# Performance work log

Measured on AMD Instinct MI355X. Metric: run time of the kernel, lower is better.

Reference implementation:

```python
import jax, jax.numpy as jnp
import numpy as np

N_EMBD = 1024
N_HEAD = 16
B, T = 4, 2048


def setup_inputs() -> dict:
    key = jax.random.key(0)
    ks = jax.random.split(key, 4)
    s = 1.0 / np.sqrt(N_EMBD)
    return {
        "x": jax.random.normal(ks[0], (B, T, N_EMBD), dtype=jnp.float32),
        "w_attn": jax.random.normal(ks[1], (N_EMBD, 3 * N_EMBD), dtype=jnp.float32) * s,
        "b_attn": jnp.zeros((3 * N_EMBD,), dtype=jnp.float32),
        "w_proj": jax.random.normal(ks[2], (N_EMBD, N_EMBD), dtype=jnp.float32) * s,
        "b_proj": jnp.zeros((N_EMBD,), dtype=jnp.float32),
    }


def reference(x, w_attn, b_attn, w_proj, b_proj):
    Bb, Tt, C = x.shape
    H = N_HEAD
    D = C // H  # head dim
    qkv = x @ w_attn + b_attn  # [B,T,3C]
    q, k, v = jnp.split(qkv, 3, axis=2)
    # [B,H,T,D]
    q = q.reshape(Bb, Tt, H, D).transpose(0, 2, 1, 3)
    k = k.reshape(Bb, Tt, H, D).transpose(0, 2, 1, 3)
    v = v.reshape(Bb, Tt, H, D).transpose(0, 2, 1, 3)
    scale = 1.0 / np.sqrt(D).astype(np.float32)
    attn = jnp.einsum("bhqd,bhkd->bhqk", q, k) * scale
    mask = jnp.tril(jnp.ones((Tt, Tt), dtype=bool))
    attn = jnp.where(mask, attn, jnp.float32(-jnp.inf))
    probs = jax.nn.softmax(attn, axis=-1)
    out = jnp.einsum("bhqk,bhkd->bhqd", probs, v)
    out = out.transpose(0, 2, 1, 3).reshape(Bb, Tt, C)
    return out @ w_proj + b_proj
```

## Files before the change

kernel.cpp:

```cpp
#include <hip/hip_runtime.h>
#include <hip/hip_bf16.h>


typedef float f32x4 __attribute__((ext_vector_type(4)));
typedef float f32x16 __attribute__((ext_vector_type(16)));
typedef short short8 __attribute__((ext_vector_type(8)));
typedef short short4v __attribute__((ext_vector_type(4)));

__device__ __forceinline__ short f2bf(float f) {
  union { __hip_bfloat16 h; short s; } u;
  u.h = __float2bfloat16(f);
  return u.s;
}

__device__ __forceinline__ void gl_lds16(const void* g, void* l) {
  __builtin_amdgcn_global_load_lds(
      (const __attribute__((address_space(1))) void*)g,
      (__attribute__((address_space(3))) void*)l, 16, 0, 0);
}

__global__ void prep(const float* __restrict__ x, const float* __restrict__ wa,
                     const float* __restrict__ wp, short* __restrict__ xb,
                     short* __restrict__ wat, short* __restrict__ wpt) {
  const int bid = blockIdx.x, tid = threadIdx.x;
  if (bid < 8192) {
    int i = (bid * 256 + tid) * 4;
    float4 v = *(const float4*)(x + i);
    short4v o;
    o[0] = f2bf(v.x); o[1] = f2bf(v.y); o[2] = f2bf(v.z); o[3] = f2bf(v.w);
    *(short4v*)(xb + i) = o;
    return;
  }
  __shared__ float tile[32][33];
  const float* in;
  short* out;
  int N, bx, by;
  if (bid < 11264) {
    int t = bid - 8192;
    in = wa; out = wat; N = 3072; bx = t % 96; by = t / 96;
  } else {
    int t = bid - 11264;
    in = wp; out = wpt; N = 1024; bx = t & 31; by = t >> 5;
  }
  int tx = tid & 31, ty = tid >> 5;
  int x0 = bx * 32, y0 = by * 32;
#pragma unroll
  for (int i = 0; i < 32; i += 8)
    tile[ty + i][tx] = in[(size_t)(y0 + ty + i) * N + x0 + tx];
  __syncthreads();
#pragma unroll
  for (int i = 0; i < 32; i += 8)
    out[(size_t)(x0 + ty + i) * 1024 + y0 + tx] = f2bf(tile[tx][ty + i]);
}

#define GEMM_BODY(A_, Bt_)                                                        \
  __shared__ __align__(16) short As[128 * 32];                                    \
  __shared__ __align__(16) short Bs[128 * 32];                                    \
  const int tid = threadIdx.x;                                                    \
  const int wv = tid >> 6;                                                        \
  const int wr = wv >> 1, wc = wv & 1;                                            \
  const int col = tid & 31, khalf = (tid >> 5) & 1;                               \
  const int m0 = blockIdx.y * 128, n0 = blockIdx.x * 128;                         \
  f32x16 acc[2][2];                                                               \
  _Pragma("unroll") for (int i = 0; i < 2; ++i)                                   \
      _Pragma("unroll") for (int j = 0; j < 2; ++j)                               \
          acc[i][j] = (f32x16)(0.f);                                              \
  for (int k0 = 0; k0 < 1024; k0 += 32) {                                         \
    _Pragma("unroll") for (int i = 0; i < 2; ++i) {                               \
      int cc = tid + i * 256;                                                     \
      int row = cc >> 2, part = ((cc & 3) - ((cc >> 3) & 3)) & 3;                 \
      gl_lds16(A_ + (size_t)(m0 + row) * 1024 + k0 + part * 8,                    \
               (char*)As + cc * 16);                                              \
      gl_lds16(Bt_ + (size_t)(n0 + row) * 1024 + k0 + part * 8,                   \
               (char*)Bs + cc * 16);                                              \
    }                                                                             \
    __syncthreads();                                                              \
    short8 af[2][2], bf[2][2];                                                    \
    _Pragma("unroll") for (int i = 0; i < 2; ++i)                                 \
        _Pragma("unroll") for (int s = 0; s < 2; ++s) {                           \
          int pa = s * 2 + khalf;                                                 \
          int ra = wr * 64 + i * 32 + col;                                        \
          int rb = wc * 64 + i * 32 + col;                                        \
          af[i][s] = *(const short8*)&As[(ra * 4 + ((pa + (ra >> 1)) & 3)) * 8];  \
          bf[i][s] = *(const short8*)&Bs[(rb * 4 + ((pa + (rb >> 1)) & 3)) * 8];  \
        }                                                                         \
    _Pragma("unroll") for (int s = 0; s < 2; ++s)                                 \
        _Pragma("unroll") for (int i = 0; i < 2; ++i)                             \
            _Pragma("unroll") for (int j = 0; j < 2; ++j)                         \
                acc[i][j] = __builtin_amdgcn_mfma_f32_32x32x16_bf16(              \
                    af[i][s], bf[j][s], acc[i][j], 0, 0, 0);                      \
    __syncthreads();                                                              \
  }

__global__ __launch_bounds__(256, 2) void gemm_proj(
    const short* __restrict__ A, const short* __restrict__ Bt,
    const float* __restrict__ bias, float* __restrict__ out) {
  GEMM_BODY(A, Bt)
  const int rhalf = khalf * 4;
#pragma unroll
  for (int i = 0; i < 2; ++i) {
#pragma unroll
    for (int j = 0; j < 2; ++j) {
      int n = n0 + wc * 64 + j * 32 + col;
      float bv = bias[n];
      int mb = m0 + wr * 64 + i * 32 + rhalf;
#pragma unroll
      for (int a = 0; a < 16; ++a) {
        int m = mb + (a & 3) + 8 * (a >> 2);
        out[(size_t)m * 1024 + n] = acc[i][j][a] + bv;
      }
    }
  }
}


#define BARRIER() asm volatile("s_barrier" ::: "memory")
#define VMC(N) asm volatile("s_waitcnt vmcnt(" #N ")" ::: "memory")

#define STG(KT, S, SRC, LB)                                                \
  if ((KT) < 16) {                                                         \
    char* db_ = (char*)(LB) + (((KT) & 1) ? 32768 : 0) + ((S) * 16384);    \
    const short* sb_ = (SRC) + (KT) * 64 + (S) * 32;                       \
    gl_lds16(sb_ + g_off0, db_ + d_off0);                                  \
    gl_lds16(sb_ + g_off1, db_ + d_off1);                                  \
  }

#define LDF(AF, BF, ABP, BBP, S, AO, BO)                                   \
  _Pragma("unroll") for (int mt_ = 0; mt_ < 4; ++mt_)                      \
      AF[mt_] = *(const short8*)((ABP) + (S) * 16384 + (AO)[mt_]);         \
  _Pragma("unroll") for (int nt_ = 0; nt_ < 2; ++nt_)                      \
      BF[nt_] = *(const short8*)((BBP) + (S) * 16384 + (BO)[nt_]);

#define MFMA8_BODY(AF, BF)                                                 \
  __builtin_amdgcn_s_setprio(1);                                           \
  _Pragma("unroll") for (int mt_ = 0; mt_ < 4; ++mt_)                      \
      _Pragma("unroll") for (int nt_ = 0; nt_ < 2; ++nt_)                  \
          acc[mt_][nt_] = __builtin_amdgcn_mfma_f32_32x32x16_bf16(         \
              AF[mt_], BF[nt_], acc[mt_][nt_], 0, 0, 0);                   \
  __builtin_amdgcn_s_setprio(0);

#define MFMA8(AF, BF)                                                      \
  __builtin_amdgcn_sched_barrier(0);                                       \
  asm volatile("s_waitcnt lgkmcnt(6)" ::: "memory");                       \
  MFMA8_BODY(AF, BF)

#define MFMA8_LG0(AF, BF)                                                  \
  __builtin_amdgcn_sched_barrier(0);                                       \
  asm volatile("s_waitcnt lgkmcnt(0)" ::: "memory");                       \
  MFMA8_BODY(AF, BF)

__global__ __launch_bounds__(512, 2) void gemm_qkv(
    const short* __restrict__ A, const short* __restrict__ Bt,
    const float* __restrict__ bias, short* __restrict__ Qb,
    short* __restrict__ Kb, short* __restrict__ Vtb) {
  __shared__ __align__(16) short Asm[2][16384];
  __shared__ __align__(16) short Bsm[2][16384];
  const int tid = threadIdx.x;
  const int wv = tid >> 6;
  const int wr = wv >> 2, wc = wv & 3;
  const int ln32 = tid & 31, khalf = (tid >> 5) & 1;
  const int m0 = blockIdx.y * 256, n0 = blockIdx.x * 256;

  const int d_off0 = tid * 16, d_off1 = d_off0 + 8192;
  const int pa_st = ((tid & 3) - ((tid >> 3) & 3)) & 3;
  const size_t g_off0 = (size_t)(tid >> 2) * 1024 + (size_t)pa_st * 8;
  const size_t g_off1 = g_off0 + (size_t)128 * 1024;

  const int rot = (ln32 >> 1) & 3;
  const int slotE = (khalf + rot) & 3;
  const int slotO = (2 + khalf + rot) & 3;
  int aoffE[4], aoffO[4], boffE[2], boffO[2];
#pragma unroll
  for (int mt = 0; mt < 4; ++mt) {
    int r = (wr * 128 + mt * 32 + ln32) * 64;
    aoffE[mt] = r + slotE * 16;
    aoffO[mt] = r + slotO * 16;
  }
#pragma unroll
  for (int nt = 0; nt < 2; ++nt) {
    int r = (wc * 64 + nt * 32 + ln32) * 64;
    boffE[nt] = r + slotE * 16;
    boffO[nt] = r + slotO * 16;
  }

  const short* srcA = A + (size_t)m0 * 1024;
  const short* srcB = Bt + (size_t)n0 * 1024;

  f32x16 acc[4][2];
#pragma unroll
  for (int i = 0; i < 4; ++i)
#pragma unroll
    for (int j = 0; j < 2; ++j) acc[i][j] = (f32x16)(0.f);

  short8 af0[4], af1[4], bf0[2], bf1[2];

  STG(0, 0, srcA, Asm)
  STG(0, 0, srcB, Bsm)
  STG(0, 1, srcA, Asm)
  STG(0, 1, srcB, Bsm)
  STG(1, 0, srcA, Asm)
  STG(1, 0, srcB, Bsm)
  VMC(4);
  BARRIER();
  {
    const char* Ab0 = (const char*)Asm;
    const char* Bb0 = (const char*)Bsm;
    LDF(af0, bf0, Ab0, Bb0, 0, aoffE, boffE)
  }

  for (int kt = 0; kt < 16; ++kt) {
    const char* Ab = (const char*)Asm + ((kt & 1) << 15);
    const char* Bb = (const char*)Bsm + ((kt & 1) << 15);
    const char* An = (const char*)Asm + (((kt + 1) & 1) << 15);
    const char* Bn = (const char*)Bsm + (((kt + 1) & 1) << 15);
    LDF(af1, bf1, Ab, Bb, 0, aoffO, boffO)
    STG(kt + 1, 1, srcA, Asm)
    MFMA8(af0, bf0)
    LDF(af0, bf0, Ab, Bb, 1, aoffE, boffE)
    STG(kt + 1, 1, srcB, Bsm)
    MFMA8(af1, bf1)
    if (kt == 15) { VMC(0); } else { VMC(4); }
    BARRIER();
    LDF(af1, bf1, Ab, Bb, 1, aoffO, boffO)
    STG(kt + 2, 0, srcA, Asm)
    MFMA8(af0, bf0)
    if (kt < 15) {
      LDF(af0, bf0, An, Bn, 0, aoffE, boffE)
      STG(kt + 2, 0, srcB, Bsm)
      MFMA8(af1, bf1)
      if (kt == 14) { VMC(0); } else { VMC(4); }
    } else {
      MFMA8_LG0(af1, bf1)
    }
    BARRIER();
  }

  const int col = tid & 31;
  const int rhalf = khalf * 4;
#pragma unroll
  for (int i = 0; i < 4; ++i) {
#pragma unroll
    for (int j = 0; j < 2; ++j) {
      int n = n0 + wc * 64 + j * 32 + col;
      int n2 = n & 1023;
      int hh = n2 >> 6, d = n2 & 63;
      float bv = bias[n];
      int mb = m0 + wr * 128 + i * 32 + rhalf;
      int bb = mb >> 11;
      int bh = (bb << 4) + hh;
      if (n < 2048) {
        const bool isq = n < 1024;
#pragma unroll
        for (int a = 0; a < 16; ++a) {
          int t = (mb + (a & 3) + 8 * (a >> 2)) & 2047;
          float o = acc[i][j][a] + bv;
          size_t idx = ((size_t)bh * 2048 + t) * 64 + d;
          if (isq)
            Qb[idx] = f2bf(o * 0.18033688f);
          else
            Kb[idx] = f2bf(o);
        }
      } else {
#pragma unroll
        for (int g = 0; g < 4; ++g) {
          int t = (mb + 8 * g) & 2047;
          short4v o;
#pragma unroll
          for (int r = 0; r < 4; ++r) o[r] = f2bf(acc[i][j][g * 4 + r] + bv);
          *(short4v*)&Vtb[((size_t)bh * 64 + d) * 2048 + t] = o;
        }
      }
    }
  }
}

__global__ __launch_bounds__(256, 2) void flash_attn(
    const short* __restrict__ Qg_, const short* __restrict__ Kg_,
    const short* __restrict__ Vg_, short* __restrict__ Ob) {
  constexpr int STR = 72;
  __shared__ __align__(16) short Kl[2][64 * STR];
  __shared__ __align__(16) short Vl[2][64 * STR];
  const int tid = threadIdx.x;
  const int wv = tid >> 6, ln = tid & 15, quad = (tid & 63) >> 4;
  const int bh = blockIdx.x & 63;
  const int pair = blockIdx.x >> 6;
  const short* Qg = Qg_ + (size_t)bh * 2048 * 64;
  const short* Kg = Kg_ + (size_t)bh * 2048 * 64;
  const short* Vg = Vg_ + (size_t)bh * 64 * 2048;
  const int srow = tid >> 3, spart = tid & 7;
  const int bb = bh >> 4, hh = bh & 15;

  short8 kreg[2], vreg[2];

#define LOADKV(KT)                                                              \
  {                                                                             \
    const short* Kt = Kg + (size_t)(KT) * 64 * 64;                              \
    _Pragma("unroll") for (int i = 0; i < 2; ++i) {                             \
      kreg[i] = *(const short8*)(Kt + (size_t)(srow + i * 32) * 64 + spart * 8);\
      vreg[i] = *(const short8*)(Vg + (size_t)(srow + i * 32) * 2048 +          \
                                 (KT) * 64 + spart * 8);                        \
    }                                                                           \
  }
#define WRITEKV(BUF)                                                            \
  _Pragma("unroll") for (int i = 0; i < 2; ++i) {                               \
    *(short8*)&Kl[BUF][(srow + i * 32) * STR + spart * 8] = kreg[i];            \
    *(short8*)&Vl[BUF][(srow + i * 32) * STR + spart * 8] = vreg[i];            \
  }

#pragma unroll
  for (int it = 0; it < 2; ++it) {
    const int qt = it ? pair : (15 - pair);
    const int q0 = qt * 128;
    const int qbase = q0 + wv * 32;
    const int nkt = (q0 >> 6) + 2;

    short8 qf[2][2];
#pragma unroll
    for (int h = 0; h < 2; ++h)
#pragma unroll
      for (int ch = 0; ch < 2; ++ch)
        qf[h][ch] = *(const short8*)(Qg + (size_t)(qbase + h * 16 + ln) * 64 +
                                     ch * 32 + quad * 8);

    f32x4 Oacc[2][4];
#pragma unroll
    for (int h = 0; h < 2; ++h)
#pragma unroll
      for (int mt = 0; mt < 4; ++mt) Oacc[h][mt] = (f32x4){0.f, 0.f, 0.f, 0.f};
    float lpart[2] = {0.f, 0.f};

    LOADKV(0)
    __syncthreads();
    WRITEKV(0)
    LOADKV(1)

    for (int kt = 0; kt < nkt; ++kt) {
      __syncthreads();
      const short* Kcur = Kl[kt & 1];
      const short* Vcur = Vl[kt & 1];
      if (kt + 1 < nkt) {
        WRITEKV((kt + 1) & 1)
        if (kt + 2 < nkt) LOADKV(kt + 2)
      }

      if (kt * 64 <= qbase + 31) {
        f32x4 St[2][4];
#pragma unroll
        for (int h = 0; h < 2; ++h)
#pragma unroll
          for (int kb = 0; kb < 4; ++kb) St[h][kb] = (f32x4){0.f, 0.f, 0.f, 0.f};
        __builtin_amdgcn_s_setprio(1);
#pragma unroll
        for (int kb = 0; kb < 4; ++kb) {
          short8 ka0 = *(const short8*)&Kcur[(kb * 16 + ln) * STR + quad * 8];
          short8 ka1 = *(const short8*)&Kcur[(kb * 16 + ln) * STR + 32 + quad * 8];
#pragma unroll
          for (int h = 0; h < 2; ++h) {
            St[h][kb] = __builtin_amdgcn_mfma_f32_16x16x32_bf16(
                ka0, qf[h][0], St[h][kb], 0, 0, 0);
            St[h][kb] = __builtin_amdgcn_mfma_f32_16x16x32_bf16(
                ka1, qf[h][1], St[h][kb], 0, 0, 0);
          }
        }
        __builtin_amdgcn_s_setprio(0);

        short4v pf[2][4];
#pragma unroll
        for (int h = 0; h < 2; ++h) {
          float lp0 = 0.f, lp1 = 0.f;
          if (kt * 64 + 63 <= qbase + h * 16) {
#pragma unroll
            for (int kb = 0; kb < 4; ++kb) {
              float p[4];
#pragma unroll
              for (int r = 0; r < 4; ++r)
                p[r] = __builtin_amdgcn_exp2f(St[h][kb][r]);
              lp0 += p[0] + p[2];
              lp1 += p[1] + p[3];
              union { __hip_bfloat162 b2; unsigned u; } w0, w1;
              w0.b2 = __float22bfloat162_rn(make_float2(p[0], p[1]));
              w1.b2 = __float22bfloat162_rn(make_float2(p[2], p[3]));
              union { short4v s4; unsigned u2[2]; } m;
              m.u2[0] = w0.u; m.u2[1] = w1.u;
              pf[h][kb] = m.s4;
            }
          } else {
            const int qg = qbase + h * 16 + ln;
#pragma unroll
            for (int kb = 0; kb < 4; ++kb) {
              float p[4];
#pragma unroll
              for (int r = 0; r < 4; ++r) {
                int key = kt * 64 + kb * 16 + quad * 4 + r;
                float s = (key <= qg) ? St[h][kb][r] : -1e30f;
                p[r] = __builtin_amdgcn_exp2f(s);
              }
              lp0 += p[0] + p[2];
              lp1 += p[1] + p[3];
              union { __hip_bfloat162 b2; unsigned u; } w0, w1;
              w0.b2 = __float22bfloat162_rn(make_float2(p[0], p[1]));
              w1.b2 = __float22bfloat162_rn(make_float2(p[2], p[3]));
              union { short4v s4; unsigned u2[2]; } m;
              m.u2[0] = w0.u; m.u2[1] = w1.u;
              pf[h][kb] = m.s4;
            }
          }
          lpart[h] += lp0 + lp1;
        }

        __builtin_amdgcn_s_setprio(1);
#pragma unroll
        for (int kb = 0; kb < 4; ++kb)
#pragma unroll
          for (int mt = 0; mt < 4; ++mt) {
            short4v va =
                *(const short4v*)&Vcur[(mt * 16 + ln) * STR + kb * 16 + quad * 4];
#pragma unroll
            for (int h = 0; h < 2; ++h)
              Oacc[h][mt] = __builtin_amdgcn_mfma_f32_16x16x16bf16_1k(
                  va, pf[h][kb], Oacc[h][mt], 0, 0, 0);
          }
        __builtin_amdgcn_s_setprio(0);
      }
    }

#pragma unroll
    for (int h = 0; h < 2; ++h) {
      float l = lpart[h];
      l += __shfl_xor(l, 16);
      l += __shfl_xor(l, 32);
      float rl = 1.0f / l;
      int t = qbase + h * 16 + ln;
#pragma unroll
      for (int mt = 0; mt < 4; ++mt) {
        short4v o;
#pragma unroll
        for (int r = 0; r < 4; ++r) o[r] = f2bf(Oacc[h][mt][r] * rl);
        *(short4v*)(Ob + ((size_t)(bb * 2048 + t)) * 1024 + hh * 64 + mt * 16 +
                    quad * 4) = o;
      }
    }
  }
#undef LOADKV
#undef WRITEKV
}


extern "C" void kernel_launch(void* const* d_in, const int* in_sizes, int n_in,
                              void* d_out, int out_size, void* d_ws, size_t ws_size,
                              hipStream_t stream) {
  const float* x      = (const float*)d_in[0];
  const float* w_attn = (const float*)d_in[1];
  const float* b_attn = (const float*)d_in[2];
  const float* w_proj = (const float*)d_in[3];
  const float* b_proj = (const float*)d_in[4];
  float* out = (float*)d_out;
  char* ws = (char*)d_ws;

  short* xb  = (short*)(ws);
  short* wat = (short*)(ws + 16777216);
  short* wpt = (short*)(ws + 23068672);
  short* Qb  = (short*)(ws + 25165824);
  short* Kb  = (short*)(ws + 41943040);
  short* Vtb = (short*)(ws + 58720256);
  short* Ob  = (short*)(ws + 75497472);

  prep<<<12288, 256, 0, stream>>>(x, w_attn, w_proj, xb, wat, wpt);
  gemm_qkv<<<dim3(12, 32), 512, 0, stream>>>(xb, wat, b_attn, Qb, Kb, Vtb);
  flash_attn<<<512, 256, 0, stream>>>(Qb, Kb, Vtb, Ob);
  gemm_proj<<<dim3(8, 64), 256, 0, stream>>>(Ob, wpt, b_proj, out);
}
```

Measured before the change: 255.5 us.

## Replace fine-grained LDS/MFMA interleave with bulk load then 16-MFMA phases

Restructures the QKV GEMM main loop so that each half-tile loads all A/B fragments at once, waits for the full LDS queue, then issues 16 MFMAs, adding extra barriers between phases. This replaces the previous software-pipelined interleave of LDS reads with MFMA groups and changes the vmcnt waits accordingly. The intent is to simplify scheduling and reduce waitcnt stalls, but it gives up overlap of LDS reads with MFMA work and adds barriers. It also holds twice as many fragment registers live at once.

```diff
diff --git a/kernel.cpp b/kernel.cpp
--- a/kernel.cpp
+++ b/kernel.cpp
@@ -125,29 +125,26 @@
     gl_lds16(sb_ + g_off1, db_ + d_off1);                                  \
   }
 
-#define LDF(AF, BF, ABP, BBP, S, AO, BO)                                   \
-  _Pragma("unroll") for (int mt_ = 0; mt_ < 4; ++mt_)                      \
-      AF[mt_] = *(const short8*)((ABP) + (S) * 16384 + (AO)[mt_]);         \
-  _Pragma("unroll") for (int nt_ = 0; nt_ < 2; ++nt_)                      \
-      BF[nt_] = *(const short8*)((BBP) + (S) * 16384 + (BO)[nt_]);
-
-#define MFMA8_BODY(AF, BF)                                                 \
+#define LDF2(S)                                                            \
+  _Pragma("unroll") for (int mt_ = 0; mt_ < 4; ++mt_) {                    \
+    af[mt_][0] = *(const short8*)(Ab + (S)*16384 + aoffE[mt_]);            \
+    af[mt_][1] = *(const short8*)(Ab + (S)*16384 + aoffO[mt_]);            \
+  }                                                                        \
+  _Pragma("unroll") for (int nt_ = 0; nt_ < 2; ++nt_) {                    \
+    bf[nt_][0] = *(const short8*)(Bb + (S)*16384 + boffE[nt_]);            \
+    bf[nt_][1] = *(const short8*)(Bb + (S)*16384 + boffO[nt_]);            \
+  }
+
+#define MFMA16()                                                           \
+  asm volatile("s_waitcnt lgkmcnt(0)" ::: "memory");                       \
+  __builtin_amdgcn_sched_barrier(0);                                       \
   __builtin_amdgcn_s_setprio(1);                                           \
-  _Pragma("unroll") for (int mt_ = 0; mt_ < 4; ++mt_)                      \
-      _Pragma("unroll") for (int nt_ = 0; nt_ < 2; ++nt_)                  \
-          acc[mt_][nt_] = __builtin_amdgcn_mfma_f32_32x32x16_bf16(         \
-              AF[mt_], BF[nt_], acc[mt_][nt_], 0, 0, 0);                   \
+  _Pragma("unroll") for (int p_ = 0; p_ < 2; ++p_)                         \
+      _Pragma("unroll") for (int mt_ = 0; mt_ < 4; ++mt_)                  \
+          _Pragma("unroll") for (int nt_ = 0; nt_ < 2; ++nt_)              \
+              acc[mt_][nt_] = __builtin_amdgcn_mfma_f32_32x32x16_bf16(     \
+                  af[mt_][p_], bf[nt_][p_], acc[mt_][nt_], 0, 0, 0);       \
   __builtin_amdgcn_s_setprio(0);
-
-#define MFMA8(AF, BF)                                                      \
-  __builtin_amdgcn_sched_barrier(0);                                       \
-  asm volatile("s_waitcnt lgkmcnt(6)" ::: "memory");                       \
-  MFMA8_BODY(AF, BF)
-
-#define MFMA8_LG0(AF, BF)                                                  \
-  __builtin_amdgcn_sched_barrier(0);                                       \
-  asm volatile("s_waitcnt lgkmcnt(0)" ::: "memory");                       \
-  MFMA8_BODY(AF, BF)
 
 __global__ __launch_bounds__(512, 2) void gemm_qkv(
     const short* __restrict__ A, const short* __restrict__ Bt,
@@ -192,7 +189,7 @@
 #pragma unroll
     for (int j = 0; j < 2; ++j) acc[i][j] = (f32x16)(0.f);
 
-  short8 af0[4], af1[4], bf0[2], bf1[2];
+  short8 af[4][2], bf[2][2];
 
   STG(0, 0, srcA, Asm)
   STG(0, 0, srcB, Bsm)
@@ -200,38 +197,25 @@
   STG(0, 1, srcB, Bsm)
   STG(1, 0, srcA, Asm)
   STG(1, 0, srcB, Bsm)
-  VMC(4);
+  VMC(8);
   BARRIER();
-  {
-    const char* Ab0 = (const char*)Asm;
-    const char* Bb0 = (const char*)Bsm;
-    LDF(af0, bf0, Ab0, Bb0, 0, aoffE, boffE)
-  }
 
   for (int kt = 0; kt < 16; ++kt) {
     const char* Ab = (const char*)Asm + ((kt & 1) << 15);
     const char* Bb = (const char*)Bsm + ((kt & 1) << 15);
-    const char* An = (const char*)Asm + (((kt + 1) & 1) << 15);
-    const char* Bn = (const char*)Bsm + (((kt + 1) & 1) << 15);
-    LDF(af1, bf1, Ab, Bb, 0, aoffO, boffO)
+    LDF2(0)
     STG(kt + 1, 1, srcA, Asm)
-    MFMA8(af0, bf0)
-    LDF(af0, bf0, Ab, Bb, 1, aoffE, boffE)
     STG(kt + 1, 1, srcB, Bsm)
-    MFMA8(af1, bf1)
-    if (kt == 15) { VMC(0); } else { VMC(4); }
     BARRIER();
-    LDF(af1, bf1, Ab, Bb, 1, aoffO, boffO)
+    MFMA16()
+    if (kt == 15) { VMC(0); } else { VMC(8); }
+    BARRIER();
+    LDF2(1)
     STG(kt + 2, 0, srcA, Asm)
-    MFMA8(af0, bf0)
-    if (kt < 15) {
-      LDF(af0, bf0, An, Bn, 0, aoffE, boffE)
-      STG(kt + 2, 0, srcB, Bsm)
-      MFMA8(af1, bf1)
-      if (kt == 14) { VMC(0); } else { VMC(4); }
-    } else {
-      MFMA8_LG0(af1, bf1)
-    }
+    STG(kt + 2, 0, srcB, Bsm)
+    BARRIER();
+    MFMA16()
+    if (kt == 14) { VMC(4); } else if (kt < 14) { VMC(8); }
     BARRIER();
   }
 
```

New measurement: 257.8 us. About the same (+0.9%).

## Rewrite flash attention as LDS-free single-wave blocks with pre-swizzled V layout

Applied to the files above, without the earlier changes.

The attention kernel now launches one 64-thread wave per 32-query tile. Each wave reads K and a V tensor stored in MFMA fragment order directly from global memory, so the LDS staging, barriers and the two-tiles-per-block loop are gone. The QKV GEMM epilogue writes V in that fragment-ordered layout. The proj GEMM also gets double-buffered LDS, which overlaps the next K-slice load with compute. The trade-off is that every wave reloads K/V from global or L2 with no sharing across waves, and there are many more small blocks.

```diff
diff --git a/kernel.cpp b/kernel.cpp
--- a/kernel.cpp
+++ b/kernel.cpp
@@ -54,35 +54,49 @@
 }
 
 #define GEMM_BODY(A_, Bt_)                                                        \
-  __shared__ __align__(16) short As[128 * 32];                                    \
-  __shared__ __align__(16) short Bs[128 * 32];                                    \
+  __shared__ __align__(16) short As[2][128 * 32];                                 \
+  __shared__ __align__(16) short Bs[2][128 * 32];                                 \
   const int tid = threadIdx.x;                                                    \
   const int wv = tid >> 6;                                                        \
   const int wr = wv >> 1, wc = wv & 1;                                            \
   const int col = tid & 31, khalf = (tid >> 5) & 1;                               \
   const int m0 = blockIdx.y * 128, n0 = blockIdx.x * 128;                         \
+  const int cc0 = tid, cc1 = tid + 256;                                           \
+  const int row0 = cc0 >> 2, part0 = ((cc0 & 3) - ((cc0 >> 3) & 3)) & 3;          \
+  const int row1 = cc1 >> 2, part1 = ((cc1 & 3) - ((cc1 >> 3) & 3)) & 3;          \
+  const size_t ga0 = (size_t)(m0 + row0) * 1024 + part0 * 8;                      \
+  const size_t ga1 = (size_t)(m0 + row1) * 1024 + part1 * 8;                      \
+  const size_t gb0 = (size_t)(n0 + row0) * 1024 + part0 * 8;                      \
+  const size_t gb1 = (size_t)(n0 + row1) * 1024 + part1 * 8;                      \
   f32x16 acc[2][2];                                                               \
   _Pragma("unroll") for (int i = 0; i < 2; ++i)                                   \
       _Pragma("unroll") for (int j = 0; j < 2; ++j)                               \
           acc[i][j] = (f32x16)(0.f);                                              \
-  for (int k0 = 0; k0 < 1024; k0 += 32) {                                         \
-    _Pragma("unroll") for (int i = 0; i < 2; ++i) {                               \
-      int cc = tid + i * 256;                                                     \
-      int row = cc >> 2, part = ((cc & 3) - ((cc >> 3) & 3)) & 3;                 \
-      gl_lds16(A_ + (size_t)(m0 + row) * 1024 + k0 + part * 8,                    \
-               (char*)As + cc * 16);                                              \
-      gl_lds16(Bt_ + (size_t)(n0 + row) * 1024 + k0 + part * 8,                   \
-               (char*)Bs + cc * 16);                                              \
+  gl_lds16(A_ + ga0, (char*)As[0] + cc0 * 16);                                    \
+  gl_lds16(A_ + ga1, (char*)As[0] + cc1 * 16);                                    \
+  gl_lds16(Bt_ + gb0, (char*)Bs[0] + cc0 * 16);                                   \
+  gl_lds16(Bt_ + gb1, (char*)Bs[0] + cc1 * 16);                                   \
+  __syncthreads();                                                                \
+  for (int kt = 0; kt < 32; ++kt) {                                               \
+    if (kt + 1 < 32) {                                                            \
+      const int k0 = (kt + 1) * 32;                                               \
+      char* Ad = (char*)As[(kt + 1) & 1];                                         \
+      char* Bd = (char*)Bs[(kt + 1) & 1];                                         \
+      gl_lds16(A_ + ga0 + k0, Ad + cc0 * 16);                                     \
+      gl_lds16(A_ + ga1 + k0, Ad + cc1 * 16);                                     \
+      gl_lds16(Bt_ + gb0 + k0, Bd + cc0 * 16);                                    \
+      gl_lds16(Bt_ + gb1 + k0, Bd + cc1 * 16);                                    \
     }                                                                             \
-    __syncthreads();                                                              \
+    const short* Ac = As[kt & 1];                                                 \
+    const short* Bc = Bs[kt & 1];                                                 \
     short8 af[2][2], bf[2][2];                                                    \
     _Pragma("unroll") for (int i = 0; i < 2; ++i)                                 \
         _Pragma("unroll") for (int s = 0; s < 2; ++s) {                           \
           int pa = s * 2 + khalf;                                                 \
           int ra = wr * 64 + i * 32 + col;                                        \
           int rb = wc * 64 + i * 32 + col;                                        \
-          af[i][s] = *(const short8*)&As[(ra * 4 + ((pa + (ra >> 1)) & 3)) * 8];  \
-          bf[i][s] = *(const short8*)&Bs[(rb * 4 + ((pa + (rb >> 1)) & 3)) * 8];  \
+          af[i][s] = *(const short8*)&Ac[(ra * 4 + ((pa + (ra >> 1)) & 3)) * 8];  \
+          bf[i][s] = *(const short8*)&Bc[(rb * 4 + ((pa + (rb >> 1)) & 3)) * 8];  \
         }                                                                         \
     _Pragma("unroll") for (int s = 0; s < 2; ++s)                                 \
         _Pragma("unroll") for (int i = 0; i < 2; ++i)                             \
@@ -112,7 +126,6 @@
     }
   }
 }
-
 
 #define BARRIER() asm volatile("s_barrier" ::: "memory")
 #define VMC(N) asm volatile("s_waitcnt vmcnt(" #N ")" ::: "memory")
@@ -261,188 +274,151 @@
             Kb[idx] = f2bf(o);
         }
       } else {
+        const int lnv = d & 15, mtv = d >> 4;
 #pragma unroll
         for (int g = 0; g < 4; ++g) {
-          int t = (mb + 8 * g) & 2047;
+          int t0 = (mb + 8 * g) & 2047;
+          int ktv = t0 >> 6, kbv = (t0 >> 4) & 3, qv = (t0 >> 2) & 3;
           short4v o;
 #pragma unroll
           for (int r = 0; r < 4; ++r) o[r] = f2bf(acc[i][j][g * 4 + r] + bv);
-          *(short4v*)&Vtb[((size_t)bh * 64 + d) * 2048 + t] = o;
+          *(short4v*)&Vtb[(size_t)(((bh * 32 + ktv) * 4 + kbv) * 4 + mtv) * 256 +
+                          (qv * 16 + lnv) * 4] = o;
         }
       }
     }
   }
 }
 
-__global__ __launch_bounds__(256, 2) void flash_attn(
+__global__ __launch_bounds__(64, 4) void flash_attn(
     const short* __restrict__ Qg_, const short* __restrict__ Kg_,
-    const short* __restrict__ Vg_, short* __restrict__ Ob) {
-  constexpr int STR = 72;
-  __shared__ __align__(16) short Kl[2][64 * STR];
-  __shared__ __align__(16) short Vl[2][64 * STR];
+    const short* __restrict__ V4_, short* __restrict__ Ob) {
   const int tid = threadIdx.x;
-  const int wv = tid >> 6, ln = tid & 15, quad = (tid & 63) >> 4;
+  const int ln = tid & 15, quad = (tid >> 4) & 3;
+  const int lane = tid;
   const int bh = blockIdx.x & 63;
-  const int pair = blockIdx.x >> 6;
+  const int c = 63 - (blockIdx.x >> 6);
+  const int qbase = c * 32;
+  const int nkt = (c >> 1) + 1;
   const short* Qg = Qg_ + (size_t)bh * 2048 * 64;
   const short* Kg = Kg_ + (size_t)bh * 2048 * 64;
-  const short* Vg = Vg_ + (size_t)bh * 64 * 2048;
-  const int srow = tid >> 3, spart = tid & 7;
+  const short* V4 = V4_ + (size_t)bh * 131072;
   const int bb = bh >> 4, hh = bh & 15;
 
-  short8 kreg[2], vreg[2];
-
-#define LOADKV(KT)                                                              \
-  {                                                                             \
-    const short* Kt = Kg + (size_t)(KT) * 64 * 64;                              \
-    _Pragma("unroll") for (int i = 0; i < 2; ++i) {                             \
-      kreg[i] = *(const short8*)(Kt + (size_t)(srow + i * 32) * 64 + spart * 8);\
-      vreg[i] = *(const short8*)(Vg + (size_t)(srow + i * 32) * 2048 +          \
-                                 (KT) * 64 + spart * 8);                        \
-    }                                                                           \
-  }
-#define WRITEKV(BUF)                                                            \
-  _Pragma("unroll") for (int i = 0; i < 2; ++i) {                               \
-    *(short8*)&Kl[BUF][(srow + i * 32) * STR + spart * 8] = kreg[i];            \
-    *(short8*)&Vl[BUF][(srow + i * 32) * STR + spart * 8] = vreg[i];            \
-  }
-
-#pragma unroll
-  for (int it = 0; it < 2; ++it) {
-    const int qt = it ? pair : (15 - pair);
-    const int q0 = qt * 128;
-    const int qbase = q0 + wv * 32;
-    const int nkt = (q0 >> 6) + 2;
-
-    short8 qf[2][2];
+  short8 qf[2][2];
+#pragma unroll
+  for (int h = 0; h < 2; ++h)
+#pragma unroll
+    for (int ch = 0; ch < 2; ++ch)
+      qf[h][ch] = *(const short8*)(Qg + (size_t)(qbase + h * 16 + ln) * 64 +
+                                   ch * 32 + quad * 8);
+
+  f32x4 Oacc[2][4];
+#pragma unroll
+  for (int h = 0; h < 2; ++h)
+#pragma unroll
+    for (int mt = 0; mt < 4; ++mt) Oacc[h][mt] = (f32x4){0.f, 0.f, 0.f, 0.f};
+  float lpart[2] = {0.f, 0.f};
+
+  for (int kt = 0; kt < nkt; ++kt) {
+    const short* Kt = Kg + (size_t)kt * 4096;
+    const short* Vt = V4 + (size_t)kt * 4096;
+
+    f32x4 St[2][4];
 #pragma unroll
     for (int h = 0; h < 2; ++h)
 #pragma unroll
-      for (int ch = 0; ch < 2; ++ch)
-        qf[h][ch] = *(const short8*)(Qg + (size_t)(qbase + h * 16 + ln) * 64 +
-                                     ch * 32 + quad * 8);
-
-    f32x4 Oacc[2][4];
-#pragma unroll
-    for (int h = 0; h < 2; ++h)
-#pragma unroll
-      for (int mt = 0; mt < 4; ++mt) Oacc[h][mt] = (f32x4){0.f, 0.f, 0.f, 0.f};
-    float lpart[2] = {0.f, 0.f};
-
-    LOADKV(0)
-    __syncthreads();
-    WRITEKV(0)
-    LOADKV(1)
-
-    for (int kt = 0; kt < nkt; ++kt) {
-      __syncthreads();
-      const short* Kcur = Kl[kt & 1];
-      const short* Vcur = Vl[kt & 1];
-      if (kt + 1 < nkt) {
-        WRITEKV((kt + 1) & 1)
-        if (kt + 2 < nkt) LOADKV(kt + 2)
+      for (int kb = 0; kb < 4; ++kb) St[h][kb] = (f32x4){0.f, 0.f, 0.f, 0.f};
+    __builtin_amdgcn_s_setprio(1);
+#pragma unroll
+    for (int kb = 0; kb < 4; ++kb) {
+      short8 ka0 = *(const short8*)(Kt + (kb * 16 + ln) * 64 + quad * 8);
+      short8 ka1 = *(const short8*)(Kt + (kb * 16 + ln) * 64 + 32 + quad * 8);
+#pragma unroll
+      for (int h = 0; h < 2; ++h) {
+        St[h][kb] = __builtin_amdgcn_mfma_f32_16x16x32_bf16(ka0, qf[h][0],
+                                                            St[h][kb], 0, 0, 0);
+        St[h][kb] = __builtin_amdgcn_mfma_f32_16x16x32_bf16(ka1, qf[h][1],
+                                                            St[h][kb], 0, 0, 0);
       }
-
-      if (kt * 64 <= qbase + 31) {
-        f32x4 St[2][4];
+    }
+    __builtin_amdgcn_s_setprio(0);
+
+    short4v pf[2][4];
+#pragma unroll
+    for (int h = 0; h < 2; ++h) {
+      float lp0 = 0.f, lp1 = 0.f;
+      if (kt * 64 + 63 <= qbase + h * 16) {
+#pragma unroll
+        for (int kb = 0; kb < 4; ++kb) {
+          float p[4];
+#pragma unroll
+          for (int r = 0; r < 4; ++r)
+            p[r] = __builtin_amdgcn_exp2f(St[h][kb][r]);
+          lp0 += p[0] + p[2];
+          lp1 += p[1] + p[3];
+          union { __hip_bfloat162 b2; unsigned u; } w0, w1;
+          w0.b2 = __float22bfloat162_rn(make_float2(p[0], p[1]));
+          w1.b2 = __float22bfloat162_rn(make_float2(p[2], p[3]));
+          union { short4v s4; unsigned u2[2]; } mm;
+          mm.u2[0] = w0.u; mm.u2[1] = w1.u;
+          pf[h][kb] = mm.s4;
+        }
+      } else {
+        const int qg = qbase + h * 16 + ln;
+#pragma unroll
+        for (int kb = 0; kb < 4; ++kb) {
+          float p[4];
+#pragma unroll
+          for (int r = 0; r < 4; ++r) {
+            int key = kt * 64 + kb * 16 + quad * 4 + r;
+            float s = (key <= qg) ? St[h][kb][r] : -1e30f;
+            p[r] = __builtin_amdgcn_exp2f(s);
+          }
+          lp0 += p[0] + p[2];
+          lp1 += p[1] + p[3];
+          union { __hip_bfloat162 b2; unsigned u; } w0, w1;
+          w0.b2 = __float22bfloat162_rn(make_float2(p[0], p[1]));
+          w1.b2 = __float22bfloat162_rn(make_float2(p[2], p[3]));
+          union { short4v s4; unsigned u2[2]; } mm;
+          mm.u2[0] = w0.u; mm.u2[1] = w1.u;
+          pf[h][kb] = mm.s4;
+        }
+      }
+      lpart[h] += lp0 + lp1;
+    }
+
+    __builtin_amdgcn_s_setprio(1);
+#pragma unroll
+    for (int kb = 0; kb < 4; ++kb) {
+#pragma unroll
+      for (int mt = 0; mt < 4; ++mt) {
+        short4v va = *(const short4v*)(Vt + (kb * 4 + mt) * 256 + lane * 4);
 #pragma unroll
         for (int h = 0; h < 2; ++h)
-#pragma unroll
-          for (int kb = 0; kb < 4; ++kb) St[h][kb] = (f32x4){0.f, 0.f, 0.f, 0.f};
-        __builtin_amdgcn_s_setprio(1);
-#pragma unroll
-        for (int kb = 0; kb < 4; ++kb) {
-          short8 ka0 = *(const short8*)&Kcur[(kb * 16 + ln) * STR + quad * 8];
-          short8 ka1 = *(const short8*)&Kcur[(kb * 16 + ln) * STR + 32 + quad * 8];
-#pragma unroll
-          for (int h = 0; h < 2; ++h) {
-            St[h][kb] = __builtin_amdgcn_mfma_f32_16x16x32_bf16(
-                ka0, qf[h][0], St[h][kb], 0, 0, 0);
-            St[h][kb] = __builtin_amdgcn_mfma_f32_16x16x32_bf16(
-                ka1, qf[h][1], St[h][kb], 0, 0, 0);
-          }
-        }
-        __builtin_amdgcn_s_setprio(0);
-
-        short4v pf[2][4];
-#pragma unroll
-        for (int h = 0; h < 2; ++h) {
-          float lp0 = 0.f, lp1 = 0.f;
-          if (kt * 64 + 63 <= qbase + h * 16) {
-#pragma unroll
-            for (int kb = 0; kb < 4; ++kb) {
-              float p[4];
-#pragma unroll
-              for (int r = 0; r < 4; ++r)
-                p[r] = __builtin_amdgcn_exp2f(St[h][kb][r]);
-              lp0 += p[0] + p[2];
-              lp1 += p[1] + p[3];
-              union { __hip_bfloat162 b2; unsigned u; } w0, w1;
-              w0.b2 = __float22bfloat162_rn(make_float2(p[0], p[1]));
-              w1.b2 = __float22bfloat162_rn(make_float2(p[2], p[3]));
-              union { short4v s4; unsigned u2[2]; } m;
-              m.u2[0] = w0.u; m.u2[1] = w1.u;
-              pf[h][kb] = m.s4;
-            }
-          } else {
-            const int qg = qbase + h * 16 + ln;
-#pragma unroll
-            for (int kb = 0; kb < 4; ++kb) {
-              float p[4];
-#pragma unroll
-              for (int r = 0; r < 4; ++r) {
-                int key = kt * 64 + kb * 16 + quad * 4 + r;
-                float s = (key <= qg) ? St[h][kb][r] : -1e30f;
-                p[r] = __builtin_amdgcn_exp2f(s);
-              }
-              lp0 += p[0] + p[2];
-              lp1 += p[1] + p[3];
-              union { __hip_bfloat162 b2; unsigned u; } w0, w1;
-              w0.b2 = __float22bfloat162_rn(make_float2(p[0], p[1]));
-              w1.b2 = __float22bfloat162_rn(make_float2(p[2], p[3]));
-              union { short4v s4; unsigned u2[2]; } m;
-              m.u2[0] = w0.u; m.u2[1] = w1.u;
-              pf[h][kb] = m.s4;
-            }
-          }
-          lpart[h] += lp0 + lp1;
-        }
-
-        __builtin_amdgcn_s_setprio(1);
-#pragma unroll
-        for (int kb = 0; kb < 4; ++kb)
-#pragma unroll
-          for (int mt = 0; mt < 4; ++mt) {
-            short4v va =
-                *(const short4v*)&Vcur[(mt * 16 + ln) * STR + kb * 16 + quad * 4];
-#pragma unroll
-            for (int h = 0; h < 2; ++h)
-              Oacc[h][mt] = __builtin_amdgcn_mfma_f32_16x16x16bf16_1k(
-                  va, pf[h][kb], Oacc[h][mt], 0, 0, 0);
-          }
-        __builtin_amdgcn_s_setprio(0);
+          Oacc[h][mt] = __builtin_amdgcn_mfma_f32_16x16x16bf16_1k(
+              va, pf[h][kb], Oacc[h][mt], 0, 0, 0);
       }
     }
-
-#pragma unroll
-    for (int h = 0; h < 2; ++h) {
-      float l = lpart[h];
-      l += __shfl_xor(l, 16);
-      l += __shfl_xor(l, 32);
-      float rl = 1.0f / l;
-      int t = qbase + h * 16 + ln;
-#pragma unroll
-      for (int mt = 0; mt < 4; ++mt) {
-        short4v o;
-#pragma unroll
-        for (int r = 0; r < 4; ++r) o[r] = f2bf(Oacc[h][mt][r] * rl);
-        *(short4v*)(Ob + ((size_t)(bb * 2048 + t)) * 1024 + hh * 64 + mt * 16 +
-                    quad * 4) = o;
-      }
-    }
-  }
-#undef LOADKV
-#undef WRITEKV
+    __builtin_amdgcn_s_setprio(0);
+  }
+
+#pragma unroll
+  for (int h = 0; h < 2; ++h) {
+    float l = lpart[h];
+    l += __shfl_xor(l, 16);
+    l += __shfl_xor(l, 32);
+    float rl = 1.0f / l;
+    int t = qbase + h * 16 + ln;
+#pragma unroll
+    for (int mt = 0; mt < 4; ++mt) {
+      short4v o;
+#pragma unroll
+      for (int r = 0; r < 4; ++r) o[r] = f2bf(Oacc[h][mt][r] * rl);
+      *(short4v*)(Ob + ((size_t)(bb * 2048 + t)) * 1024 + hh * 64 + mt * 16 +
+                  quad * 4) = o;
+    }
+  }
 }
 
 
@@ -467,6 +443,6 @@
 
   prep<<<12288, 256, 0, stream>>>(x, w_attn, w_proj, xb, wat, wpt);
   gemm_qkv<<<dim3(12, 32), 512, 0, stream>>>(xb, wat, b_attn, Qb, Kb, Vtb);
-  flash_attn<<<512, 256, 0, stream>>>(Qb, Kb, Vtb, Ob);
+  flash_attn<<<4096, 64, 0, stream>>>(Qb, Kb, Vtb, Ob);
   gemm_proj<<<dim3(8, 64), 256, 0, stream>>>(Ob, wpt, b_proj, out);
 }
```

Measured after the change: 294.5 us. 1.15x slower.
